# Optimization experiments

Hardware: AMD Instinct MI355X
Metric: run time of the kernel (lower is better)

Reference implementation:

```python
import jax, jax.numpy as jnp
import numpy as np

SIGMA = 0.001
EPS_LOG = 1e-12
EPS_COS = 1e-8


def setup_inputs() -> dict:
    key = jax.random.key(0)
    k1, k2, k3, k4 = jax.random.split(key, 4)
    B, T, K, S, d = 32, 512, 8, 8, 300
    center_pos = jax.random.randint(k1, (B,), 0, T)
    query_token_ids = jax.random.randint(k2, (B, T), 0, 30000)
    center_sense_embeddings = jax.random.normal(k3, (B, K, d), dtype=jnp.float32)
    context_sense_embeddings = jax.random.normal(k4, (B, T - 1, S, d), dtype=jnp.float32)
    return {
        'center_pos': center_pos,
        'query_token_ids': query_token_ids,
        'center_sense_embeddings': center_sense_embeddings,
        'context_sense_embeddings': context_sense_embeddings,
    }


def reference(center_pos, query_token_ids, center_sense_embeddings, context_sense_embeddings):
    B, T = query_token_ids.shape
    d = center_sense_embeddings.shape[-1]
    # v: mean over senses of context tokens -> [B, C, d], C = T-1
    v = context_sense_embeddings.mean(axis=-2)
    # a: scaled dot between center senses and context vectors -> [B, C, K]
    a = jnp.einsum('bkd,bcd->bck', center_sense_embeddings, v) / jnp.sqrt(jnp.float32(d))
    # context positions: skip the center position (vectorized form of the per-batch loop)
    i = jnp.arange(T - 1)  # [C]
    ctx_pos = i[None, :] + (i[None, :] >= center_pos[:, None])  # [B, C]
    w = jnp.exp(-jnp.abs(ctx_pos - center_pos[:, None]).astype(jnp.float32) / SIGMA)
    logw = jnp.log(jnp.maximum(w, EPS_LOG))  # [B, C]
    alpha = jax.nn.softmax(a + logw[:, :, None], axis=1)  # softmax over context positions
    m = jnp.einsum('bck,bcd->bkd', alpha, v)  # [B, K, d]
    # cosine similarity along d (torch semantics: clamp each norm by eps)
    num = jnp.sum(center_sense_embeddings * m, axis=-1)
    n1 = jnp.linalg.norm(center_sense_embeddings, axis=-1)
    n2 = jnp.linalg.norm(m, axis=-1)
    s = num / (jnp.maximum(n1, EPS_COS) * jnp.maximum(n2, EPS_COS))  # [B, K]
    q = jax.nn.softmax(s, axis=-1)
    idx = jnp.argmax(q, axis=-1)  # [B]
    pooled = jnp.take_along_axis(center_sense_embeddings, idx[:, None, None], axis=1)[:, 0, :]  # [B, d]
    return pooled, q
```

## Files before the change

### kernel.cpp

```cpp
#include <hip/hip_runtime.h>

#define NB 32
#define NC 511
#define NK 8
#define NS 8
#define ND 300
#define ND4 75
#define NCG 32
#define CPB 16
#define EPS_COS 1e-8f


typedef float nfloat4 __attribute__((ext_vector_type(4)));

__device__ __forceinline__ void n4add(nfloat4& a, const nfloat4& b) { a += b; }

__global__ __launch_bounds__(512) void k_vam(const float* __restrict__ ctx,
                                             const float* __restrict__ cen,
                                             float* __restrict__ part) {
    const int b    = blockIdx.x >> 5;
    const int cg   = blockIdx.x & 31;
    const int w    = threadIdx.x >> 6;
    const int lane = threadIdx.x & 63;
    const int i0 = lane;
    const int i1 = lane + 64;
    const bool has1 = (i1 < ND4);

    const nfloat4* cen4 = (const nfloat4*)cen + (size_t)b * NK * ND4;

    nfloat4 macc0[NK] = {};
    nfloat4 macc1[NK] = {};

#pragma unroll
    for (int cc = 0; cc < 2; ++cc) {
        const int c = cg * CPB + 2 * w + cc;
        if (c >= NC) break;

        const nfloat4* ctx4 = (const nfloat4*)ctx + (size_t)(b * NC + c) * NS * ND4;

        nfloat4 X[NS];
#pragma unroll
        for (int s = 0; s < NS; ++s)
            X[s] = __builtin_nontemporal_load(&ctx4[s * ND4 + i0]);
        nfloat4 Y[NS] = {};
        if (has1) {
#pragma unroll
            for (int s = 0; s < NS; ++s)
                Y[s] = __builtin_nontemporal_load(&ctx4[s * ND4 + i1]);
        }

        n4add(X[0], X[1]); n4add(X[2], X[3]); n4add(X[4], X[5]); n4add(X[6], X[7]);
        n4add(X[0], X[2]); n4add(X[4], X[6]);
        n4add(X[0], X[4]);
        n4add(Y[0], Y[1]); n4add(Y[2], Y[3]); n4add(Y[4], Y[5]); n4add(Y[6], Y[7]);
        n4add(Y[0], Y[2]); n4add(Y[4], Y[6]);
        n4add(Y[0], Y[4]);
        const float inv = 0.125f;
        nfloat4 s0 = X[0] * inv;
        nfloat4 s1 = Y[0] * inv;

        float pk[NK];
#pragma unroll
        for (int k = 0; k < NK; ++k) {
            nfloat4 ca = cen4[k * ND4 + i0];
            float p = ca.x * s0.x + ca.y * s0.y + ca.z * s0.z + ca.w * s0.w;
            if (has1) {
                nfloat4 cb = cen4[k * ND4 + i1];
                p += cb.x * s1.x + cb.y * s1.y + cb.z * s1.z + cb.w * s1.w;
            }
            pk[k] = p;
        }

        const bool b0 = (lane & 1) != 0;
        float r[4];
#pragma unroll
        for (int j = 0; j < 4; ++j) {
            float keep = b0 ? pk[2 * j + 1] : pk[2 * j];
            float send = b0 ? pk[2 * j]     : pk[2 * j + 1];
            r[j] = keep + __shfl_xor(send, 1);
        }
        const bool b1 = (lane & 2) != 0;
        float q0, q1;
        { float keep = b1 ? r[1] : r[0]; float send = b1 ? r[0] : r[1];
          q0 = keep + __shfl_xor(send, 2); }
        { float keep = b1 ? r[3] : r[2]; float send = b1 ? r[2] : r[3];
          q1 = keep + __shfl_xor(send, 2); }
        const bool b2 = (lane & 4) != 0;
        float u;
        { float keep = b2 ? q1 : q0; float send = b2 ? q0 : q1;
          u = keep + __shfl_xor(send, 4); }
        u += __shfl_xor(u, 8);
        u += __shfl_xor(u, 16);
        u += __shfl_xor(u, 32);

        const float scale = 0.057735026919f;
        float e = __expf(u * scale);

        float eav[NK];
#pragma unroll
        for (int k = 0; k < NK; ++k) eav[k] = __shfl(e, k);

#pragma unroll
        for (int k = 0; k < NK; ++k) {
            macc0[k] += eav[k] * s0;
            macc1[k] += eav[k] * s1;
        }
    }

    __shared__ float pl[8][NK][ND4 * 4 + 4];
#pragma unroll
    for (int k = 0; k < NK; ++k) {
        ((nfloat4*)pl[w][k])[i0] = macc0[k];
        if (has1) ((nfloat4*)pl[w][k])[i1] = macc1[k];
    }
    __syncthreads();

    for (int idx = threadIdx.x; idx < NK * ND; idx += 512) {
        const int k = idx / ND;
        const int d = idx - k * ND;
        float s = 0.f;
#pragma unroll
        for (int ww = 0; ww < 8; ++ww) s += pl[ww][k][d];
        part[(((size_t)b * NK + k) * NCG + cg) * ND + d] = s;
    }
}

__global__ __launch_bounds__(512) void k_fin2(const float* __restrict__ part,
                                              const float* __restrict__ cen,
                                              float* __restrict__ out) {
    const int b    = blockIdx.x;
    const int w    = threadIdx.x >> 6;
    const int lane = threadIdx.x & 63;
    __shared__ float sred[NK];
    __shared__ int bidx;

    const float* pp = part + ((size_t)b * NK + w) * NCG * ND;
    const float* cp = cen + (size_t)(b * NK + w) * ND;
    float num = 0.f, n1 = 0.f, n2 = 0.f;
    for (int d = lane; d < ND; d += 64) {
        float mval = 0.f;
#pragma unroll
        for (int cg = 0; cg < NCG; ++cg) mval += pp[cg * ND + d];
        float cv = cp[d];
        num += cv * mval; n1 += cv * cv; n2 += mval * mval;
    }
#pragma unroll
    for (int off = 32; off; off >>= 1) {
        num += __shfl_down(num, off);
        n1  += __shfl_down(n1, off);
        n2  += __shfl_down(n2, off);
    }
    if (lane == 0) {
        float denom = fmaxf(sqrtf(n1), EPS_COS) * fmaxf(sqrtf(n2), EPS_COS);
        sred[w] = num / denom;
    }
    __syncthreads();

    if (threadIdx.x == 0) {
        float mx = sred[0];
#pragma unroll
        for (int k = 1; k < NK; ++k) mx = fmaxf(mx, sred[k]);
        float e[NK], sum = 0.f;
#pragma unroll
        for (int k = 0; k < NK; ++k) { e[k] = __expf(sred[k] - mx); sum += e[k]; }
        float invs = 1.f / sum;
        int best = 0; float bv = sred[0];
#pragma unroll
        for (int k = 1; k < NK; ++k) if (sred[k] > bv) { bv = sred[k]; best = k; }
#pragma unroll
        for (int k = 0; k < NK; ++k)
            out[(size_t)NB * ND + b * NK + k] = e[k] * invs;
        bidx = best;
    }
    __syncthreads();

    const float* src = cen + (size_t)(b * NK + bidx) * ND;
    for (int idx = threadIdx.x; idx < ND; idx += 512)
        out[(size_t)b * ND + idx] = src[idx];
}

extern "C" void kernel_launch(void* const* d_in, const int* in_sizes, int n_in,
                              void* d_out, int out_size, void* d_ws, size_t ws_size,
                              hipStream_t stream) {
    const float* cen = (const float*)d_in[2];
    const float* ctx = (const float*)d_in[3];
    float* out = (float*)d_out;

    float* part = (float*)d_ws;

    k_vam<<<dim3(NB * NCG), dim3(512), 0, stream>>>(ctx, cen, part);
    k_fin2<<<dim3(NB), dim3(512), 0, stream>>>(part, cen, out);
}
```

Before: 257.2 us.

## Restructure context reduction to stage means and weights through shared memory

Each block now has 256 threads and covers 32 contexts in 8 groups of 4, instead of 512 threads covering 16 contexts. Each wave computes one context's sense mean and exp-weights and stages them in LDS. After a barrier, every thread accumulates all 8 senses for its own d-columns in scalar registers. This removes the 64-register vec4 accumulators and the final 8-way LDS reduction across waves. The cost is two barriers per group, one context load in flight per wave at a time, and half as many partial groups, which lowers memory-level parallelism.

```diff
diff --git a/kernel.cpp b/kernel.cpp
--- a/kernel.cpp
+++ b/kernel.cpp
@@ -6,8 +6,8 @@
 #define NS 8
 #define ND 300
 #define ND4 75
-#define NCG 32
-#define CPB 16
+#define NCG 16
+#define GPB 8
 #define EPS_COS 1e-8f
 
 
@@ -15,113 +15,124 @@
 
 __device__ __forceinline__ void n4add(nfloat4& a, const nfloat4& b) { a += b; }
 
-__global__ __launch_bounds__(512) void k_vam(const float* __restrict__ ctx,
-                                             const float* __restrict__ cen,
-                                             float* __restrict__ part) {
-    const int b    = blockIdx.x >> 5;
-    const int cg   = blockIdx.x & 31;
+__global__ __launch_bounds__(256, 4) void k_vam(const float* __restrict__ ctx,
+                                                const float* __restrict__ cen,
+                                                float* __restrict__ part) {
+    const int b    = blockIdx.x >> 4;
+    const int cg   = blockIdx.x & 15;
     const int w    = threadIdx.x >> 6;
     const int lane = threadIdx.x & 63;
+    const int t    = threadIdx.x;
     const int i0 = lane;
     const int i1 = lane + 64;
-    const bool has1 = (i1 < ND4);
+    const bool has1  = (i1 < ND4);
+    const bool hasd1 = (t < ND - 256);
+
+    __shared__ float vl[4][ND4 * 4 + 4];
+    __shared__ float al[4][NK];
 
     const nfloat4* cen4 = (const nfloat4*)cen + (size_t)b * NK * ND4;
 
-    nfloat4 macc0[NK] = {};
-    nfloat4 macc1[NK] = {};
-
-#pragma unroll
-    for (int cc = 0; cc < 2; ++cc) {
-        const int c = cg * CPB + 2 * w + cc;
-        if (c >= NC) break;
-
-        const nfloat4* ctx4 = (const nfloat4*)ctx + (size_t)(b * NC + c) * NS * ND4;
-
-        nfloat4 X[NS];
-#pragma unroll
-        for (int s = 0; s < NS; ++s)
-            X[s] = __builtin_nontemporal_load(&ctx4[s * ND4 + i0]);
-        nfloat4 Y[NS] = {};
-        if (has1) {
+    float acc0[NK] = {};
+    float acc1[NK] = {};
+
+    const int cbase0 = cg * 32;
+
+    for (int g = 0; g < GPB; ++g) {
+        const int cbase = cbase0 + g * 4;
+        const int cn = min(4, NC - cbase);
+        const int c = cbase + w;
+
+        if (c < NC) {
+            const nfloat4* ctx4 =
+                (const nfloat4*)ctx + (size_t)(b * NC + c) * NS * ND4;
+
+            nfloat4 X[NS];
 #pragma unroll
             for (int s = 0; s < NS; ++s)
-                Y[s] = __builtin_nontemporal_load(&ctx4[s * ND4 + i1]);
+                X[s] = __builtin_nontemporal_load(&ctx4[s * ND4 + i0]);
+            nfloat4 Y[NS] = {};
+            if (has1) {
+#pragma unroll
+                for (int s = 0; s < NS; ++s)
+                    Y[s] = __builtin_nontemporal_load(&ctx4[s * ND4 + i1]);
+            }
+
+            n4add(X[0], X[1]); n4add(X[2], X[3]); n4add(X[4], X[5]); n4add(X[6], X[7]);
+            n4add(X[0], X[2]); n4add(X[4], X[6]);
+            n4add(X[0], X[4]);
+            n4add(Y[0], Y[1]); n4add(Y[2], Y[3]); n4add(Y[4], Y[5]); n4add(Y[6], Y[7]);
+            n4add(Y[0], Y[2]); n4add(Y[4], Y[6]);
+            n4add(Y[0], Y[4]);
+            const float inv = 0.125f;
+            nfloat4 s0 = X[0] * inv;
+            nfloat4 s1 = Y[0] * inv;
+
+            ((nfloat4*)vl[w])[i0] = s0;
+            if (has1) ((nfloat4*)vl[w])[i1] = s1;
+
+            float pk[NK];
+#pragma unroll
+            for (int k = 0; k < NK; ++k) {
+                nfloat4 ca = cen4[k * ND4 + i0];
+                float p = ca.x * s0.x + ca.y * s0.y + ca.z * s0.z + ca.w * s0.w;
+                if (has1) {
+                    nfloat4 cb = cen4[k * ND4 + i1];
+                    p += cb.x * s1.x + cb.y * s1.y + cb.z * s1.z + cb.w * s1.w;
+                }
+                pk[k] = p;
+            }
+
+            const bool b0 = (lane & 1) != 0;
+            float r[4];
+#pragma unroll
+            for (int j = 0; j < 4; ++j) {
+                float keep = b0 ? pk[2 * j + 1] : pk[2 * j];
+                float send = b0 ? pk[2 * j]     : pk[2 * j + 1];
+                r[j] = keep + __shfl_xor(send, 1);
+            }
+            const bool b1 = (lane & 2) != 0;
+            float q0, q1;
+            { float keep = b1 ? r[1] : r[0]; float send = b1 ? r[0] : r[1];
+              q0 = keep + __shfl_xor(send, 2); }
+            { float keep = b1 ? r[3] : r[2]; float send = b1 ? r[2] : r[3];
+              q1 = keep + __shfl_xor(send, 2); }
+            const bool b2 = (lane & 4) != 0;
+            float u;
+            { float keep = b2 ? q1 : q0; float send = b2 ? q0 : q1;
+              u = keep + __shfl_xor(send, 4); }
+            u += __shfl_xor(u, 8);
+            u += __shfl_xor(u, 16);
+            u += __shfl_xor(u, 32);
+
+            if (lane < NK) {
+                const float scale = 0.057735026919f;
+                al[w][lane] = __expf(u * scale);
+            }
         }
-
-        n4add(X[0], X[1]); n4add(X[2], X[3]); n4add(X[4], X[5]); n4add(X[6], X[7]);
-        n4add(X[0], X[2]); n4add(X[4], X[6]);
-        n4add(X[0], X[4]);
-        n4add(Y[0], Y[1]); n4add(Y[2], Y[3]); n4add(Y[4], Y[5]); n4add(Y[6], Y[7]);
-        n4add(Y[0], Y[2]); n4add(Y[4], Y[6]);
-        n4add(Y[0], Y[4]);
-        const float inv = 0.125f;
-        nfloat4 s0 = X[0] * inv;
-        nfloat4 s1 = Y[0] * inv;
-
-        float pk[NK];
-#pragma unroll
-        for (int k = 0; k < NK; ++k) {
-            nfloat4 ca = cen4[k * ND4 + i0];
-            float p = ca.x * s0.x + ca.y * s0.y + ca.z * s0.z + ca.w * s0.w;
-            if (has1) {
-                nfloat4 cb = cen4[k * ND4 + i1];
-                p += cb.x * s1.x + cb.y * s1.y + cb.z * s1.z + cb.w * s1.w;
-            }
-            pk[k] = p;
+        __syncthreads();
+
+        for (int cc = 0; cc < cn; ++cc) {
+            float vv0 = vl[cc][t];
+#pragma unroll
+            for (int k = 0; k < NK; ++k) acc0[k] += al[cc][k] * vv0;
         }
-
-        const bool b0 = (lane & 1) != 0;
-        float r[4];
-#pragma unroll
-        for (int j = 0; j < 4; ++j) {
-            float keep = b0 ? pk[2 * j + 1] : pk[2 * j];
-            float send = b0 ? pk[2 * j]     : pk[2 * j + 1];
-            r[j] = keep + __shfl_xor(send, 1);
+        if (hasd1) {
+            for (int cc = 0; cc < cn; ++cc) {
+                float vv1 = vl[cc][256 + t];
+#pragma unroll
+                for (int k = 0; k < NK; ++k) acc1[k] += al[cc][k] * vv1;
+            }
         }
-        const bool b1 = (lane & 2) != 0;
-        float q0, q1;
-        { float keep = b1 ? r[1] : r[0]; float send = b1 ? r[0] : r[1];
-          q0 = keep + __shfl_xor(send, 2); }
-        { float keep = b1 ? r[3] : r[2]; float send = b1 ? r[2] : r[3];
-          q1 = keep + __shfl_xor(send, 2); }
-        const bool b2 = (lane & 4) != 0;
-        float u;
-        { float keep = b2 ? q1 : q0; float send = b2 ? q0 : q1;
-          u = keep + __shfl_xor(send, 4); }
-        u += __shfl_xor(u, 8);
-        u += __shfl_xor(u, 16);
-        u += __shfl_xor(u, 32);
-
-        const float scale = 0.057735026919f;
-        float e = __expf(u * scale);
-
-        float eav[NK];
-#pragma unroll
-        for (int k = 0; k < NK; ++k) eav[k] = __shfl(e, k);
-
-#pragma unroll
-        for (int k = 0; k < NK; ++k) {
-            macc0[k] += eav[k] * s0;
-            macc1[k] += eav[k] * s1;
-        }
-    }
-
-    __shared__ float pl[8][NK][ND4 * 4 + 4];
+        __syncthreads();
+        asm volatile("" ::: "memory");
+    }
+
 #pragma unroll
     for (int k = 0; k < NK; ++k) {
-        ((nfloat4*)pl[w][k])[i0] = macc0[k];
-        if (has1) ((nfloat4*)pl[w][k])[i1] = macc1[k];
-    }
-    __syncthreads();
-
-    for (int idx = threadIdx.x; idx < NK * ND; idx += 512) {
-        const int k = idx / ND;
-        const int d = idx - k * ND;
-        float s = 0.f;
-#pragma unroll
-        for (int ww = 0; ww < 8; ++ww) s += pl[ww][k][d];
-        part[(((size_t)b * NK + k) * NCG + cg) * ND + d] = s;
+        float* pp = part + (((size_t)(b * NK + k)) * NCG + cg) * ND;
+        pp[t] = acc0[k];
+        if (hasd1) pp[256 + t] = acc1[k];
     }
 }
 
@@ -188,6 +199,6 @@
 
     float* part = (float*)d_ws;
 
-    k_vam<<<dim3(NB * NCG), dim3(512), 0, stream>>>(ctx, cen, part);
+    k_vam<<<dim3(NB * NCG), dim3(256), 0, stream>>>(ctx, cen, part);
     k_fin2<<<dim3(NB), dim3(512), 0, stream>>>(part, cen, out);
 }
```

New measurement: 238.7 us. 7.2% less time.

## Give each wave eight contexts and write per-wave partials directly, dropping LDS reduction

Applied to the files above, without the earlier changes.

The main kernel now launches 512 blocks of 256 threads, where each wave loops over 8 context positions instead of 2. Each wave writes its own partial accumulators straight to global memory (64 chunks per batch), replacing the shared-memory cross-wave reduction and its barrier. The aim is to cut sync and reduction overhead and to amortize the center-embedding loads over more contexts. In exchange, the loop is now serialized per wave, the partial buffer doubles in size, and the finalize kernel has to sum 64 chunks instead of 32.

```diff
diff --git a/kernel.cpp b/kernel.cpp
--- a/kernel.cpp
+++ b/kernel.cpp
@@ -6,8 +6,7 @@
 #define NS 8
 #define ND 300
 #define ND4 75
-#define NCG 32
-#define CPB 16
+#define NCH2 64
 #define EPS_COS 1e-8f
 
 
@@ -15,11 +14,11 @@
 
 __device__ __forceinline__ void n4add(nfloat4& a, const nfloat4& b) { a += b; }
 
-__global__ __launch_bounds__(512) void k_vam(const float* __restrict__ ctx,
-                                             const float* __restrict__ cen,
-                                             float* __restrict__ part) {
-    const int b    = blockIdx.x >> 5;
-    const int cg   = blockIdx.x & 31;
+__global__ __launch_bounds__(256, 2) void k_vam(const float* __restrict__ ctx,
+                                                const float* __restrict__ cen,
+                                                float* __restrict__ part) {
+    const int b    = blockIdx.x >> 4;
+    const int cg   = blockIdx.x & 15;
     const int w    = threadIdx.x >> 6;
     const int lane = threadIdx.x & 63;
     const int i0 = lane;
@@ -31,12 +30,15 @@
     nfloat4 macc0[NK] = {};
     nfloat4 macc1[NK] = {};
 
-#pragma unroll
-    for (int cc = 0; cc < 2; ++cc) {
-        const int c = cg * CPB + 2 * w + cc;
+    const int c0 = cg * 32 + w * 8;
+
+#pragma unroll 1
+    for (int ci = 0; ci < 8; ++ci) {
+        const int c = c0 + ci;
         if (c >= NC) break;
 
-        const nfloat4* ctx4 = (const nfloat4*)ctx + (size_t)(b * NC + c) * NS * ND4;
+        const nfloat4* ctx4 =
+            (const nfloat4*)ctx + (size_t)(b * NC + c) * NS * ND4;
 
         nfloat4 X[NS];
 #pragma unroll
@@ -99,29 +101,22 @@
         float eav[NK];
 #pragma unroll
         for (int k = 0; k < NK; ++k) eav[k] = __shfl(e, k);
-
 #pragma unroll
         for (int k = 0; k < NK; ++k) {
             macc0[k] += eav[k] * s0;
             macc1[k] += eav[k] * s1;
         }
+
+        asm volatile("" ::: "memory");
     }
 
-    __shared__ float pl[8][NK][ND4 * 4 + 4];
+    const int chunk = cg * 4 + w;
 #pragma unroll
     for (int k = 0; k < NK; ++k) {
-        ((nfloat4*)pl[w][k])[i0] = macc0[k];
-        if (has1) ((nfloat4*)pl[w][k])[i1] = macc1[k];
-    }
-    __syncthreads();
-
-    for (int idx = threadIdx.x; idx < NK * ND; idx += 512) {
-        const int k = idx / ND;
-        const int d = idx - k * ND;
-        float s = 0.f;
-#pragma unroll
-        for (int ww = 0; ww < 8; ++ww) s += pl[ww][k][d];
-        part[(((size_t)b * NK + k) * NCG + cg) * ND + d] = s;
+        nfloat4* pp = (nfloat4*)(part +
+            (((size_t)(b * NK + k)) * NCH2 + chunk) * ND);
+        pp[i0] = macc0[k];
+        if (has1) pp[i1] = macc1[k];
     }
 }
 
@@ -134,13 +129,13 @@
     __shared__ float sred[NK];
     __shared__ int bidx;
 
-    const float* pp = part + ((size_t)b * NK + w) * NCG * ND;
+    const float* pp = part + ((size_t)b * NK + w) * NCH2 * ND;
     const float* cp = cen + (size_t)(b * NK + w) * ND;
     float num = 0.f, n1 = 0.f, n2 = 0.f;
     for (int d = lane; d < ND; d += 64) {
         float mval = 0.f;
 #pragma unroll
-        for (int cg = 0; cg < NCG; ++cg) mval += pp[cg * ND + d];
+        for (int ch = 0; ch < NCH2; ++ch) mval += pp[ch * ND + d];
         float cv = cp[d];
         num += cv * mval; n1 += cv * cv; n2 += mval * mval;
     }
@@ -188,6 +183,6 @@
 
     float* part = (float*)d_ws;
 
-    k_vam<<<dim3(NB * NCG), dim3(512), 0, stream>>>(ctx, cen, part);
+    k_vam<<<dim3(NB * 16), dim3(256), 0, stream>>>(ctx, cen, part);
     k_fin2<<<dim3(NB), dim3(512), 0, stream>>>(part, cen, out);
 }
```

After: 242.3 us. -5.8%, faster.
